# Kernel optimization log

Measured on AMD Instinct MI355X. Metric: run time of the kernel, lower is better.

Reference implementation:

```python
import jax, jax.numpy as jnp
import numpy as np
import math

B, S, D, H = 8, 512, 768, 12
DK = D // H
NEG = 1.0e9


def _split_heads(x):
    # [B,S,D] -> [B,H,S,DK]
    b, s, d = x.shape
    return x.reshape(b, s, H, DK).transpose(0, 2, 1, 3)


def setup_inputs() -> dict:
    key = jax.random.key(0)
    ks = jax.random.split(key, 16)
    std = 1.0 / math.sqrt(D)
    query = jax.random.normal(ks[0], (B, S, D), jnp.float32)
    key_t = jax.random.normal(ks[1], (B, S, D), jnp.float32)
    # mask: 0 for valid tokens, -10000 sentinel for padding
    mask = jnp.where(jax.random.bernoulli(ks[2], 0.9, (B, S)), 0.0, -10000.0).astype(jnp.float32)
    # span targets: binary [H,B,S,S]
    span_matrix = jax.random.bernoulli(ks[3], 0.1, (H, B, S, S)).astype(jnp.float32)
    def lin(i):
        W = jax.random.normal(ks[4 + 2 * i], (D, D), jnp.float32) * std
        b = jax.random.normal(ks[5 + 2 * i], (D,), jnp.float32) * std
        return W, b
    Wql, bql = lin(0)
    Wkl, bkl = lin(1)
    Wqr, bqr = lin(2)
    Wkr, bkr = lin(3)
    Wq, bq = lin(4)
    Wk, bk = lin(5)
    return dict(query=query, key=key_t, mask=mask, span_matrix=span_matrix,
                Wql=Wql, bql=bql, Wkl=Wkl, bkl=bkl,
                Wqr=Wqr, bqr=bqr, Wkr=Wkr, bkr=bkr,
                Wq=Wq, bq=bq, Wk=Wk, bk=bk)


def _forward(query, key, mask, span_matrix,
             Wql, bql, Wkl, bkl, Wqr, bqr, Wkr, bkr, Wq, bq, Wk, bk):
    scale = 1.0 / math.sqrt(D)  # note: original scales by sqrt(model_dim), not sqrt(d_k)
    idx = jnp.arange(S)
    lower = idx[None, :] <= idx[:, None]  # [S,S] lower-triangular incl. diag
    left_boundary = jnp.where(lower, 0.0, NEG)   # 1e9 above diagonal
    right_boundary = left_boundary.T             # 1e9 below diagonal

    # left branch
    ql = _split_heads(query @ Wql + bql) * scale
    kl = _split_heads(key @ Wkl + bkl)
    left_scores = jnp.einsum('bhqd,bhkd->bhqk', ql, kl)
    theta_l = jax.nn.softmax(left_scores - left_boundary, axis=-1)

    # right branch
    qr = _split_heads(query @ Wqr + bqr) * scale
    kr = _split_heads(key @ Wkr + bkr)
    right_scores = jnp.einsum('bhqd,bhkd->bhqk', qr, kr)
    theta_r = jax.nn.softmax(right_scores - right_boundary, axis=-1)

    # theta_l @ upperTri == inclusive cumsum over last axis (O(S) instead of O(S^2) matmul)
    soft_Mask_l = jnp.cumsum(theta_l, axis=-1)
    # theta_r @ lowerTri == inclusive reverse cumsum over last axis
    soft_Mask_r = jnp.cumsum(theta_r[..., ::-1], axis=-1)[..., ::-1]
    soft_Mask = soft_Mask_l * soft_Mask_r

    # main attention
    q = _split_heads(query @ Wq + bq) * scale
    k = _split_heads(key @ Wk + bk)
    att_scores = jnp.einsum('bhqd,bhkd->bhqk', q, k)
    row_mask = jnp.where(mask == -10000.0, NEG, mask)  # [B,S]
    att_scores = att_scores - row_mask[:, None, :, None] - row_mask[:, None, None, :]
    p_local_attn = jax.nn.softmax(att_scores * soft_Mask, axis=-1)

    # per-head BCE between sigmoid(attn) and span targets; mean over heads of per-head means
    # == global mean since every head has the same element count
    span = span_matrix.transpose(1, 0, 2, 3)  # [B,H,S,S]
    p_sig = jax.nn.sigmoid(p_local_attn)      # in (0.5, 0.732], logs are safe
    bce = -(span * jnp.log(p_sig) + (1.0 - span) * jnp.log1p(-p_sig))
    span_loss = jnp.mean(bce)
    return p_local_attn, span_loss


def reference(query, key, mask, span_matrix,
              Wql, bql, Wkl, bkl, Wqr, bqr, Wkr, bkr, Wq, bq, Wk, bk):
    return _forward(query, key, mask, span_matrix,
                    Wql, bql, Wkl, bkl, Wqr, bqr, Wkr, bkr, Wq, bq, Wk, bk)
```

## Files before the change

### kernel.cpp

```cpp
#include <hip/hip_runtime.h>
#include <math.h>

#define BB 8
#define SS 512
#define DD 768
#define HH 12
#define DKK 64
#define NTOK (BB*SS)
#define NELEM (25165824ull)
#define NPROJ 3145728
#define WSZ   589824
#define SCALEQ 0.03608439182435161f

typedef unsigned short u16;
typedef short short8 __attribute__((ext_vector_type(8)));
typedef float f32x4 __attribute__((ext_vector_type(4)));
typedef unsigned short u16x4 __attribute__((ext_vector_type(4)));

#define MFMA16 __builtin_amdgcn_mfma_f32_16x16x32_bf16

__device__ inline u16 f32_to_bf16(float f) {
    unsigned int u = __float_as_uint(f);
    unsigned int r = u + 0x7fffu + ((u >> 16) & 1u);
    return (u16)(r >> 16);
}
__device__ inline float bf16_to_f32(u16 h) {
    return __uint_as_float(((unsigned int)h) << 16);
}

__device__ __forceinline__ void gld16(const u16* g, u16* l) {
    __builtin_amdgcn_global_load_lds(
        (const __attribute__((address_space(1))) unsigned int*)g,
        (__attribute__((address_space(3))) unsigned int*)l, 16, 0, 0);
}

__global__ __launch_bounds__(256)
void cast_wT(const float* __restrict__ W0, const float* __restrict__ W1,
             const float* __restrict__ W2, const float* __restrict__ W3,
             const float* __restrict__ W4, const float* __restrict__ W5,
             u16* __restrict__ WTh, u16* __restrict__ WTl,
             float* __restrict__ lossp)
{
    __shared__ float tile[32][33];
    if (blockIdx.x == 0 && blockIdx.y == 0 && blockIdx.z == 0 && threadIdx.x == 0)
        *lossp = 0.0f;
    const int z = blockIdx.z;
    const float* W;
    switch (z) {
        case 0: W = W0; break; case 1: W = W1; break; case 2: W = W2; break;
        case 3: W = W3; break; case 4: W = W4; break; default: W = W5; break;
    }
    u16* th = WTh + (size_t)z * WSZ;
    u16* tl = WTl + (size_t)z * WSZ;
    const int t = threadIdx.x;
    const int k0 = blockIdx.y * 32, n0 = blockIdx.x * 32;
    const int rr = t >> 3, c0 = (t & 7) * 4;

    float4 v = *(const float4*)(W + (size_t)(k0 + rr) * DD + n0 + c0);
    tile[rr][c0 + 0] = v.x; tile[rr][c0 + 1] = v.y;
    tile[rr][c0 + 2] = v.z; tile[rr][c0 + 3] = v.w;
    __syncthreads();

    u16x4 hw, lw;
#pragma unroll
    for (int i = 0; i < 4; ++i) {
        float f = tile[c0 + i][rr];
        u16 hi = f32_to_bf16(f);
        hw[i] = hi;
        lw[i] = f32_to_bf16(f - bf16_to_f32(hi));
    }
    size_t o = (size_t)(n0 + rr) * DD + k0 + c0;
    *(u16x4*)&th[o] = hw;
    *(u16x4*)&tl[o] = lw;
}

__global__ __launch_bounds__(256)
void cast_X(const float* __restrict__ query, const float* __restrict__ key,
            u16* __restrict__ Xh, u16* __restrict__ Xl)
{
    const float* src = blockIdx.y ? key : query;
    u16* dh = Xh + (size_t)blockIdx.y * NPROJ;
    u16* dl = Xl + (size_t)blockIdx.y * NPROJ;
    size_t i0 = ((size_t)blockIdx.x * 256 + threadIdx.x) * 8;
    float f[8];
    *(float4*)&f[0] = *(const float4*)(src + i0);
    *(float4*)&f[4] = *(const float4*)(src + i0 + 4);
    short8 h, l;
#pragma unroll
    for (int i = 0; i < 8; ++i) {
        u16 hi = f32_to_bf16(f[i]);
        h[i] = (short)hi;
        l[i] = (short)f32_to_bf16(f[i] - bf16_to_f32(hi));
    }
    *(short8*)&dh[i0] = h;
    *(short8*)&dl[i0] = l;
}

__global__ __launch_bounds__(256)
void proj_gemm_gld(const u16* __restrict__ Xh, const u16* __restrict__ Xl,
                   const u16* __restrict__ WTh, const u16* __restrict__ WTl,
                   const float* __restrict__ b0, const float* __restrict__ b1,
                   const float* __restrict__ b2, const float* __restrict__ b3,
                   const float* __restrict__ b4, const float* __restrict__ b5,
                   u16* __restrict__ Ph, u16* __restrict__ Pl)
{
    __shared__ alignas(16) u16 Ash[128][32];
    __shared__ alignas(16) u16 Asl[128][32];
    __shared__ alignas(16) u16 Bsh[128][32];
    __shared__ alignas(16) u16 Bsl[128][32];

    const int z = blockIdx.z;
    const float* bias;
    switch (z) {
        case 0: bias = b0; break; case 1: bias = b1; break; case 2: bias = b2; break;
        case 3: bias = b3; break; case 4: bias = b4; break; default: bias = b5; break;
    }
    const float scl = (z & 1) ? 1.0f : SCALEQ;
    const u16* Ah_g = Xh + (size_t)(z & 1) * NPROJ;
    const u16* Al_g = Xl + (size_t)(z & 1) * NPROJ;
    const u16* WThz = WTh + (size_t)z * WSZ;
    const u16* WTlz = WTl + (size_t)z * WSZ;
    u16* Ch = Ph + (size_t)z * NPROJ;
    u16* Cl = Pl + (size_t)z * NPROJ;
    const bool wlo = (z < 4);

    const int t = threadIdx.x;
    const int w = t >> 6, l = t & 63, quad = l >> 4, ln = l & 15;
    const int m0 = blockIdx.y * 128, n0 = blockIdx.x * 128;
    const int wm = (w & 1) * 64, wn = (w >> 1) * 64;

    const int srow = w * 16 + (l >> 2);
    const int scol = (l & 3) * 8;
    const u16* gAh = Ah_g + (size_t)(m0 + srow) * DD + scol;
    const u16* gAl = Al_g + (size_t)(m0 + srow) * DD + scol;
    const u16* gBh = WThz + (size_t)(n0 + srow) * DD + scol;
    const u16* gBl = WTlz + (size_t)(n0 + srow) * DD + scol;
    u16* lAh0 = &Ash[w * 16][0];      u16* lAh1 = &Ash[w * 16 + 64][0];
    u16* lAl0 = &Asl[w * 16][0];      u16* lAl1 = &Asl[w * 16 + 64][0];
    u16* lBh0 = &Bsh[w * 16][0];      u16* lBh1 = &Bsh[w * 16 + 64][0];
    u16* lBl0 = &Bsl[w * 16][0];      u16* lBl1 = &Bsl[w * 16 + 64][0];
    const size_t rstep = (size_t)64 * DD;

    f32x4 acc[4][4];
#pragma unroll
    for (int i = 0; i < 4; ++i)
#pragma unroll
        for (int jj = 0; jj < 4; ++jj) acc[i][jj] = (f32x4){0.f, 0.f, 0.f, 0.f};

    for (int k0 = 0; k0 < DD; k0 += 32) {
        gld16(gAh + k0, lAh0);  gld16(gAh + k0 + rstep, lAh1);
        gld16(gBh + k0, lBh0);  gld16(gBh + k0 + rstep, lBh1);
        if (wlo) {
            gld16(gAl + k0, lAl0);  gld16(gAl + k0 + rstep, lAl1);
            gld16(gBl + k0, lBl0);  gld16(gBl + k0 + rstep, lBl1);
        }
        __syncthreads();

        short8 afh[4], afl[4], bfh[4], bfl[4];
#pragma unroll
        for (int mt = 0; mt < 4; ++mt)
            afh[mt] = *(const short8*)&Ash[wm + mt * 16 + ln][quad * 8];
#pragma unroll
        for (int nt = 0; nt < 4; ++nt)
            bfh[nt] = *(const short8*)&Bsh[wn + nt * 16 + ln][quad * 8];
        if (wlo) {
#pragma unroll
            for (int mt = 0; mt < 4; ++mt)
                afl[mt] = *(const short8*)&Asl[wm + mt * 16 + ln][quad * 8];
#pragma unroll
            for (int nt = 0; nt < 4; ++nt)
                bfl[nt] = *(const short8*)&Bsl[wn + nt * 16 + ln][quad * 8];
        }
#pragma unroll
        for (int mt = 0; mt < 4; ++mt)
#pragma unroll
            for (int nt = 0; nt < 4; ++nt) {
                acc[mt][nt] = MFMA16(bfh[nt], afh[mt], acc[mt][nt], 0, 0, 0);
                if (wlo) {
                    acc[mt][nt] = MFMA16(bfl[nt], afh[mt], acc[mt][nt], 0, 0, 0);
                    acc[mt][nt] = MFMA16(bfh[nt], afl[mt], acc[mt][nt], 0, 0, 0);
                }
            }
        __syncthreads();
    }

#pragma unroll
    for (int nt = 0; nt < 4; ++nt) {
        const int nb4 = n0 + wn + nt * 16 + quad * 4;
        float4 bias4 = *(const float4*)(bias + nb4);
        float bv[4] = {bias4.x, bias4.y, bias4.z, bias4.w};
#pragma unroll
        for (int mt = 0; mt < 4; ++mt) {
            const int m = m0 + wm + mt * 16 + ln;
            u16x4 hv, lv;
#pragma unroll
            for (int reg = 0; reg < 4; ++reg) {
                float c = (acc[mt][nt][reg] + bv[reg]) * scl;
                u16 hi = f32_to_bf16(c);
                hv[reg] = hi;
                lv[reg] = f32_to_bf16(c - bf16_to_f32(hi));
            }
            size_t o = (size_t)m * DD + nb4;
            *(u16x4*)&Ch[o] = hv;
            if (wlo) *(u16x4*)&Cl[o] = lv;
        }
    }
}

__global__ __launch_bounds__(256)
void proj_gemm_mfma(const float* __restrict__ query, const float* __restrict__ key,
                    const u16* __restrict__ WTh, const u16* __restrict__ WTl,
                    const float* __restrict__ b0, const float* __restrict__ b1,
                    const float* __restrict__ b2, const float* __restrict__ b3,
                    const float* __restrict__ b4, const float* __restrict__ b5,
                    u16* __restrict__ Ph, u16* __restrict__ Pl)
{
    __shared__ alignas(16) u16 Ash[128][40];
    __shared__ alignas(16) u16 Asl[128][40];
    __shared__ alignas(16) u16 Bsh[128][40];
    __shared__ alignas(16) u16 Bsl[128][40];

    const int z = blockIdx.z;
    const float* X = (z & 1) ? key : query;
    const float* bias;
    switch (z) {
        case 0: bias = b0; break; case 1: bias = b1; break; case 2: bias = b2; break;
        case 3: bias = b3; break; case 4: bias = b4; break; default: bias = b5; break;
    }
    const float scl = (z & 1) ? 1.0f : SCALEQ;
    const u16* WThz = WTh + (size_t)z * WSZ;
    const u16* WTlz = WTl + (size_t)z * WSZ;
    u16* Ch = Ph + (size_t)z * NPROJ;
    u16* Cl = Pl + (size_t)z * NPROJ;
    const bool wlo = (z < 4);

    const int t = threadIdx.x;
    const int w = t >> 6, l = t & 63, quad = l >> 4, ln = l & 15;
    const int m0 = blockIdx.y * 128, n0 = blockIdx.x * 128;
    const int wm = (w & 1) * 64, wn = (w >> 1) * 64;

    const int arow = t >> 1, akoff = (t & 1) * 16;
    const int brow = t >> 1, bkoff = (t & 1) * 16;

    f32x4 acc[4][4];
#pragma unroll
    for (int i = 0; i < 4; ++i)
#pragma unroll
        for (int jj = 0; jj < 4; ++jj) acc[i][jj] = (f32x4){0.f, 0.f, 0.f, 0.f};

    for (int k0 = 0; k0 < DD; k0 += 32) {
        {
            const float* asrc = X + (size_t)(m0 + arow) * DD + k0 + akoff;
            float fa[16];
            *(float4*)&fa[0]  = *(const float4*)(asrc + 0);
            *(float4*)&fa[4]  = *(const float4*)(asrc + 4);
            *(float4*)&fa[8]  = *(const float4*)(asrc + 8);
            *(float4*)&fa[12] = *(const float4*)(asrc + 12);
            short8 h0, h1, l0, l1;
#pragma unroll
            for (int i = 0; i < 8; ++i) {
                u16 hi = f32_to_bf16(fa[i]);
                h0[i] = (short)hi;
                l0[i] = (short)f32_to_bf16(fa[i] - bf16_to_f32(hi));
                u16 hi2 = f32_to_bf16(fa[8 + i]);
                h1[i] = (short)hi2;
                l1[i] = (short)f32_to_bf16(fa[8 + i] - bf16_to_f32(hi2));
            }
            *(short8*)&Ash[arow][akoff]     = h0;
            *(short8*)&Ash[arow][akoff + 8] = h1;
            *(short8*)&Asl[arow][akoff]     = l0;
            *(short8*)&Asl[arow][akoff + 8] = l1;
        }
        {
            const u16* bhp = WThz + (size_t)(n0 + brow) * DD + k0 + bkoff;
            const u16* blp = WTlz + (size_t)(n0 + brow) * DD + k0 + bkoff;
            *(uint4*)&Bsh[brow][bkoff]     = *(const uint4*)(bhp);
            *(uint4*)&Bsh[brow][bkoff + 8] = *(const uint4*)(bhp + 8);
            *(uint4*)&Bsl[brow][bkoff]     = *(const uint4*)(blp);
            *(uint4*)&Bsl[brow][bkoff + 8] = *(const uint4*)(blp + 8);
        }
        __syncthreads();

        short8 afh[4], afl[4], bfh[4], bfl[4];
#pragma unroll
        for (int mt = 0; mt < 4; ++mt) {
            afh[mt] = *(const short8*)&Ash[wm + mt * 16 + ln][quad * 8];
            afl[mt] = *(const short8*)&Asl[wm + mt * 16 + ln][quad * 8];
        }
#pragma unroll
        for (int nt = 0; nt < 4; ++nt) {
            bfh[nt] = *(const short8*)&Bsh[wn + nt * 16 + ln][quad * 8];
            bfl[nt] = *(const short8*)&Bsl[wn + nt * 16 + ln][quad * 8];
        }
#pragma unroll
        for (int mt = 0; mt < 4; ++mt)
#pragma unroll
            for (int nt = 0; nt < 4; ++nt) {
                acc[mt][nt] = MFMA16(bfh[nt], afh[mt], acc[mt][nt], 0, 0, 0);
                acc[mt][nt] = MFMA16(bfl[nt], afh[mt], acc[mt][nt], 0, 0, 0);
                acc[mt][nt] = MFMA16(bfh[nt], afl[mt], acc[mt][nt], 0, 0, 0);
            }
        __syncthreads();
    }

#pragma unroll
    for (int nt = 0; nt < 4; ++nt) {
        const int nb4 = n0 + wn + nt * 16 + quad * 4;
        float4 bias4 = *(const float4*)(bias + nb4);
        float bv[4] = {bias4.x, bias4.y, bias4.z, bias4.w};
#pragma unroll
        for (int mt = 0; mt < 4; ++mt) {
            const int m = m0 + wm + mt * 16 + ln;
            u16x4 hv, lv;
#pragma unroll
            for (int reg = 0; reg < 4; ++reg) {
                float c = (acc[mt][nt][reg] + bv[reg]) * scl;
                u16 hi = f32_to_bf16(c);
                hv[reg] = hi;
                lv[reg] = f32_to_bf16(c - bf16_to_f32(hi));
            }
            size_t o = (size_t)m * DD + nb4;
            *(u16x4*)&Ch[o] = hv;
            if (wlo) *(u16x4*)&Cl[o] = lv;
        }
    }
}

__global__ __launch_bounds__(512, 8)
void attn_mfma(const u16* __restrict__ Ph, const u16* __restrict__ Pl,
               const float* __restrict__ mask, const float* __restrict__ span,
               float* __restrict__ outp, float* __restrict__ lossp)
{
    __shared__ float curb[16][516];
    __shared__ float lred[8];

    const int t = threadIdx.x;
    const int blk = blockIdx.x;
    const int qt = blk & 31;
    const int bh = blk >> 5;
    const int b = bh / HH, h = bh % HH;
    const int w = t >> 6, l = t & 63, quad = l >> 4, ln = l & 15;
    const int r = t >> 5, j = t & 31;
    const int qrow = qt * 16 + r;

    float smbr[16];

    auto compute_scores = [&](const u16* Qh, const u16* Ql,
                              const u16* Kh, const u16* Kl, bool use_lo) {
        const size_t qoff = (size_t)(b * SS + qt * 16 + ln) * DD + h * DKK + quad * 8;
        short8 ah0 = *(const short8*)(Qh + qoff);
        short8 ah1 = *(const short8*)(Qh + qoff + 32);
        short8 al0 = ah0, al1 = ah1;
        if (use_lo) {
            al0 = *(const short8*)(Ql + qoff);
            al1 = *(const short8*)(Ql + qoff + 32);
        }
        const size_t koff = (size_t)(b * SS + w * 16 + ln) * DD + h * DKK + quad * 8;
        const u16* kb = Kh + koff;
        const u16* klb = use_lo ? (Kl + koff) : kb;
        __syncthreads();
#pragma unroll
        for (int kc = 0; kc < 4; ++kc) {
            const size_t off = (size_t)kc * (128 * DD);
            short8 bh0 = *(const short8*)(kb + off);
            short8 bh1 = *(const short8*)(kb + off + 32);
            f32x4 acc = (f32x4){0.f, 0.f, 0.f, 0.f};
            acc = MFMA16(ah0, bh0, acc, 0, 0, 0);
            acc = MFMA16(ah1, bh1, acc, 0, 0, 0);
            if (use_lo) {
                short8 bl0 = *(const short8*)(klb + off);
                short8 bl1 = *(const short8*)(klb + off + 32);
                acc = MFMA16(ah0, bl0, acc, 0, 0, 0);
                acc = MFMA16(ah1, bl1, acc, 0, 0, 0);
                acc = MFMA16(al0, bh0, acc, 0, 0, 0);
                acc = MFMA16(al1, bh1, acc, 0, 0, 0);
            }
            const int cbase = kc * 128 + w * 16 + ln;
#pragma unroll
            for (int reg = 0; reg < 4; ++reg)
                curb[quad * 4 + reg][cbase] = acc[reg];
        }
        __syncthreads();
    };

    compute_scores(Ph + 0 * (size_t)NPROJ, Pl + 0 * (size_t)NPROJ,
                   Ph + 1 * (size_t)NPROJ, Pl + 1 * (size_t)NPROJ, true);
    {
        float sc[16];
        float mx = -3.0e38f;
#pragma unroll
        for (int u = 0; u < 16; ++u) {
            int c = u * 32 + j;
            float v = curb[r][c];
            sc[u] = v;
            if (c <= qrow && v > mx) mx = v;
        }
#pragma unroll
        for (int off = 16; off >= 1; off >>= 1) mx = fmaxf(mx, __shfl_xor(mx, off));
#pragma unroll
        for (int u = 0; u < 16; ++u) {
            int c = u * 32 + j;
            sc[u] = (c <= qrow) ? __expf(sc[u] - mx) : 0.0f;
        }
#pragma unroll
        for (int u = 0; u < 16; ++u) {
#pragma unroll
            for (int off = 1; off < 32; off <<= 1) {
                float ww = __shfl_up(sc[u], off, 32);
                if (j >= off) sc[u] += ww;
            }
        }
        float run = 0.0f;
#pragma unroll
        for (int u = 0; u < 16; ++u) {
            smbr[u] = run + sc[u];
            run += __shfl(sc[u], 31, 32);
        }
        float inv = 1.0f / run;
#pragma unroll
        for (int u = 0; u < 16; ++u) smbr[u] *= inv;
    }

    compute_scores(Ph + 2 * (size_t)NPROJ, Pl + 2 * (size_t)NPROJ,
                   Ph + 3 * (size_t)NPROJ, Pl + 3 * (size_t)NPROJ, true);
    {
        float sc[16];
        float mx = -3.0e38f;
#pragma unroll
        for (int u = 0; u < 16; ++u) {
            int c = u * 32 + j;
            float v = curb[r][c];
            sc[u] = v;
            if (c >= qrow && v > mx) mx = v;
        }
#pragma unroll
        for (int off = 16; off >= 1; off >>= 1) mx = fmaxf(mx, __shfl_xor(mx, off));
#pragma unroll
        for (int u = 0; u < 16; ++u) {
            int c = u * 32 + j;
            sc[u] = (c >= qrow) ? __expf(sc[u] - mx) : 0.0f;
        }
#pragma unroll
        for (int u = 0; u < 16; ++u) {
#pragma unroll
            for (int off = 1; off < 32; off <<= 1) {
                float ww = __shfl_down(sc[u], off, 32);
                if (j + off < 32) sc[u] += ww;
            }
        }
        float run = 0.0f;
#pragma unroll
        for (int u = 15; u >= 0; --u) {
            smbr[u] *= (run + sc[u]);
            run += __shfl(sc[u], 0, 32);
        }
        float inv = 1.0f / run;
#pragma unroll
        for (int u = 0; u < 16; ++u) smbr[u] *= inv;
    }

    compute_scores(Ph + 4 * (size_t)NPROJ, (const u16*)0,
                   Ph + 5 * (size_t)NPROJ, (const u16*)0, false);
    {
        float mv  = mask[b * SS + qrow];
        float rmq = (mv == -10000.0f) ? 1.0e9f : mv;
        float vb[16];
        float mx = -3.0e38f;
#pragma unroll
        for (int u = 0; u < 16; ++u) {
            int c = u * 32 + j;
            float mk  = mask[b * SS + c];
            float rmk = (mk == -10000.0f) ? 1.0e9f : mk;
            float v = (curb[r][c] - rmq - rmk) * smbr[u];
            vb[u] = v;
            mx = fmaxf(mx, v);
        }
#pragma unroll
        for (int off = 16; off >= 1; off >>= 1) mx = fmaxf(mx, __shfl_xor(mx, off));
        float sum = 0.0f;
#pragma unroll
        for (int u = 0; u < 16; ++u) {
            float ev = __expf(vb[u] - mx);
            vb[u] = ev; sum += ev;
        }
#pragma unroll
        for (int off = 16; off >= 1; off >>= 1) sum += __shfl_xor(sum, off);
        float inv = 1.0f / sum;

        float* orow = outp + (((size_t)(b * HH + h) * SS + qrow)) * SS;
        const float* sprow = span + (((size_t)(h * BB + b) * SS + qrow)) * SS;
        float lsum = 0.0f;
#pragma unroll
        for (int u = 0; u < 16; ++u) {
            int c = u * 32 + j;
            float p = vb[u] * inv;
            orow[c] = p;
            float s = sprow[c];
            lsum += __logf(1.0f + __expf(-p)) + (1.0f - s) * p;
        }
#pragma unroll
        for (int off = 32; off >= 1; off >>= 1) lsum += __shfl_xor(lsum, off);
        if ((t & 63) == 0) lred[t >> 6] = lsum;
        __syncthreads();
        if (t == 0) {
            float tot = 0.0f;
#pragma unroll
            for (int i = 0; i < 8; ++i) tot += lred[i];
            atomicAdd(lossp, tot * (float)(1.0 / 25165824.0));
        }
    }
}

extern "C" void kernel_launch(void* const* d_in, const int* in_sizes, int n_in,
                              void* d_out, int out_size, void* d_ws, size_t ws_size,
                              hipStream_t stream)
{
    const float* query = (const float*)d_in[0];
    const float* key_t = (const float*)d_in[1];
    const float* mask  = (const float*)d_in[2];
    const float* span  = (const float*)d_in[3];
    const float* Wql = (const float*)d_in[4];  const float* bql = (const float*)d_in[5];
    const float* Wkl = (const float*)d_in[6];  const float* bkl = (const float*)d_in[7];
    const float* Wqr = (const float*)d_in[8];  const float* bqr = (const float*)d_in[9];
    const float* Wkr = (const float*)d_in[10]; const float* bkr = (const float*)d_in[11];
    const float* Wq  = (const float*)d_in[12]; const float* bq  = (const float*)d_in[13];
    const float* Wk  = (const float*)d_in[14]; const float* bk  = (const float*)d_in[15];

    float* out = (float*)d_out;
    float* lossp = out + NELEM;

    u16* ws16 = (u16*)d_ws;
    u16* WTh = ws16;
    u16* WTl = WTh + (size_t)6 * WSZ;
    u16* Ph  = WTl + (size_t)6 * WSZ;
    u16* Pl  = Ph + (size_t)6 * NPROJ;
    u16* Xh  = Pl + (size_t)4 * NPROJ;
    u16* Xl  = Xh + (size_t)2 * NPROJ;
    const size_t need_big = ((size_t)12 * WSZ + (size_t)14 * NPROJ) * 2;
    const bool bigws = ws_size >= need_big;

    cast_wT<<<dim3(24, 24, 6), dim3(256), 0, stream>>>(
        Wql, Wkl, Wqr, Wkr, Wq, Wk, WTh, WTl, lossp);

    if (bigws) {
        cast_X<<<dim3(1536, 2), dim3(256), 0, stream>>>(query, key_t, Xh, Xl);
        proj_gemm_gld<<<dim3(DD / 128, NTOK / 128, 6), dim3(256), 0, stream>>>(
            Xh, Xl, WTh, WTl, bql, bkl, bqr, bkr, bq, bk, Ph, Pl);
    } else {
        proj_gemm_mfma<<<dim3(DD / 128, NTOK / 128, 6), dim3(256), 0, stream>>>(
            query, key_t, WTh, WTl, bql, bkl, bqr, bkr, bq, bk, Ph, Pl);
    }

    attn_mfma<<<dim3(96 * 32), dim3(512), 0, stream>>>(
        Ph, Pl, mask, span, out, lossp);
}
```

Before: 518.1 us.

## Use per-thread contiguous column chunks for cumsum scans with padded LDS layout

Each thread in the cumulative-sum softmax branches now owns 16 contiguous columns instead of columns strided by 32. Each thread does a serial local prefix sum, and a single warp-level shuffle scan produces the offsets, replacing the previous 16 separate 5-step shuffle scans. The LDS score buffer is padded (one extra float per 32 columns) to avoid bank conflicts under the new access pattern. The product mask is transposed back through LDS to the strided layout for the main softmax, which adds a barrier. Launch bounds occupancy hint is lowered from 8 to 4.

```diff
diff --git a/kernel.cpp b/kernel.cpp
--- a/kernel.cpp
+++ b/kernel.cpp
@@ -326,12 +326,13 @@
     }
 }
 
-__global__ __launch_bounds__(512, 8)
+#define CPITCH 532
+__global__ __launch_bounds__(512, 4)
 void attn_mfma(const u16* __restrict__ Ph, const u16* __restrict__ Pl,
                const float* __restrict__ mask, const float* __restrict__ span,
                float* __restrict__ outp, float* __restrict__ lossp)
 {
-    __shared__ float curb[16][516];
+    __shared__ float curb[16][CPITCH];
     __shared__ float lred[8];
 
     const int t = threadIdx.x;
@@ -342,6 +343,8 @@
     const int w = t >> 6, l = t & 63, quad = l >> 4, ln = l & 15;
     const int r = t >> 5, j = t & 31;
     const int qrow = qt * 16 + r;
+    const int bb = 33 * (j >> 1) + 16 * (j & 1);
+    const int cB = j * 16;
 
     float smbr[16];
 
@@ -375,10 +378,11 @@
                 acc = MFMA16(al0, bh0, acc, 0, 0, 0);
                 acc = MFMA16(al1, bh1, acc, 0, 0, 0);
             }
-            const int cbase = kc * 128 + w * 16 + ln;
+            const int cb = kc * 128 + w * 16 + ln;
+            const int ci = cb + (cb >> 5);
 #pragma unroll
             for (int reg = 0; reg < 4; ++reg)
-                curb[quad * 4 + reg][cbase] = acc[reg];
+                curb[quad * 4 + reg][ci] = acc[reg];
         }
         __syncthreads();
     };
@@ -386,77 +390,71 @@
     compute_scores(Ph + 0 * (size_t)NPROJ, Pl + 0 * (size_t)NPROJ,
                    Ph + 1 * (size_t)NPROJ, Pl + 1 * (size_t)NPROJ, true);
     {
-        float sc[16];
+        float e[16];
         float mx = -3.0e38f;
 #pragma unroll
         for (int u = 0; u < 16; ++u) {
-            int c = u * 32 + j;
-            float v = curb[r][c];
-            sc[u] = v;
-            if (c <= qrow && v > mx) mx = v;
+            float v = curb[r][bb + u];
+            e[u] = v;
+            if (cB + u <= qrow && v > mx) mx = v;
         }
 #pragma unroll
         for (int off = 16; off >= 1; off >>= 1) mx = fmaxf(mx, __shfl_xor(mx, off));
+        float s = 0.0f;
 #pragma unroll
         for (int u = 0; u < 16; ++u) {
-            int c = u * 32 + j;
-            sc[u] = (c <= qrow) ? __expf(sc[u] - mx) : 0.0f;
-        }
-#pragma unroll
-        for (int u = 0; u < 16; ++u) {
-#pragma unroll
-            for (int off = 1; off < 32; off <<= 1) {
-                float ww = __shfl_up(sc[u], off, 32);
-                if (j >= off) sc[u] += ww;
-            }
-        }
-        float run = 0.0f;
-#pragma unroll
-        for (int u = 0; u < 16; ++u) {
-            smbr[u] = run + sc[u];
-            run += __shfl(sc[u], 31, 32);
-        }
-        float inv = 1.0f / run;
-#pragma unroll
-        for (int u = 0; u < 16; ++u) smbr[u] *= inv;
+            float ev = (cB + u <= qrow) ? __expf(e[u] - mx) : 0.0f;
+            s += ev;
+            e[u] = s;
+        }
+        float incl = s;
+#pragma unroll
+        for (int off = 1; off < 32; off <<= 1) {
+            float ww = __shfl_up(incl, off, 32);
+            if (j >= off) incl += ww;
+        }
+        float offset = incl - s;
+        float inv = 1.0f / __shfl(incl, 31, 32);
+#pragma unroll
+        for (int u = 0; u < 16; ++u) smbr[u] = (offset + e[u]) * inv;
     }
 
     compute_scores(Ph + 2 * (size_t)NPROJ, Pl + 2 * (size_t)NPROJ,
                    Ph + 3 * (size_t)NPROJ, Pl + 3 * (size_t)NPROJ, true);
     {
-        float sc[16];
+        float e[16];
         float mx = -3.0e38f;
 #pragma unroll
         for (int u = 0; u < 16; ++u) {
-            int c = u * 32 + j;
-            float v = curb[r][c];
-            sc[u] = v;
-            if (c >= qrow && v > mx) mx = v;
+            float v = curb[r][bb + u];
+            e[u] = v;
+            if (cB + u >= qrow && v > mx) mx = v;
         }
 #pragma unroll
         for (int off = 16; off >= 1; off >>= 1) mx = fmaxf(mx, __shfl_xor(mx, off));
-#pragma unroll
-        for (int u = 0; u < 16; ++u) {
-            int c = u * 32 + j;
-            sc[u] = (c >= qrow) ? __expf(sc[u] - mx) : 0.0f;
-        }
-#pragma unroll
-        for (int u = 0; u < 16; ++u) {
-#pragma unroll
-            for (int off = 1; off < 32; off <<= 1) {
-                float ww = __shfl_down(sc[u], off, 32);
-                if (j + off < 32) sc[u] += ww;
-            }
-        }
-        float run = 0.0f;
+        float s = 0.0f;
 #pragma unroll
         for (int u = 15; u >= 0; --u) {
-            smbr[u] *= (run + sc[u]);
-            run += __shfl(sc[u], 0, 32);
-        }
-        float inv = 1.0f / run;
-#pragma unroll
-        for (int u = 0; u < 16; ++u) smbr[u] *= inv;
+            float ev = (cB + u >= qrow) ? __expf(e[u] - mx) : 0.0f;
+            s += ev;
+            e[u] = s;
+        }
+        float incl = s;
+#pragma unroll
+        for (int off = 1; off < 32; off <<= 1) {
+            float ww = __shfl_down(incl, off, 32);
+            if (j + off < 32) incl += ww;
+        }
+        float offset = incl - s;
+        float inv = 1.0f / __shfl(incl, 0, 32);
+#pragma unroll
+        for (int u = 0; u < 16; ++u) smbr[u] *= (offset + e[u]) * inv;
+
+#pragma unroll
+        for (int u = 0; u < 16; ++u) curb[r][bb + u] = smbr[u];
+        __syncthreads();
+#pragma unroll
+        for (int u = 0; u < 16; ++u) smbr[u] = curb[r][u * 33 + j];
     }
 
     compute_scores(Ph + 4 * (size_t)NPROJ, (const u16*)0,
@@ -471,7 +469,7 @@
             int c = u * 32 + j;
             float mk  = mask[b * SS + c];
             float rmk = (mk == -10000.0f) ? 1.0e9f : mk;
-            float v = (curb[r][c] - rmq - rmk) * smbr[u];
+            float v = (curb[r][u * 33 + j] - rmq - rmk) * smbr[u];
             vb[u] = v;
             mx = fmaxf(mx, v);
         }
```

Measured after the change: 471.6 us. 9.0% less time.
